# Kernel tuning notes

Measured on AMD Instinct MI355X. Metric: run time of the kernel, lower is better.

## Reference

```python
import jax, jax.numpy as jnp
import numpy as np

DIM = 1536
N_HEADS = 12
HEAD_DIM = DIM // N_HEADS          # 128
C = HEAD_DIM // 2                  # 64 complex channels
C_F = C - 2 * (C // 3)             # 22
C_H = C // 3                       # 21
C_W = C // 3                       # 21
EPS = 1e-6
MAX_F, MAX_HW = 64, 64


def _rope_table(max_len, c_sub):
    # Wan rope_params: theta_j = 10000^{-j/c_sub}, angle = pos * theta
    inv = 1.0 / (10000.0 ** (np.arange(c_sub, dtype=np.float32) / c_sub))
    ang = np.arange(max_len, dtype=np.float32)[:, None] * inv[None, :]
    return jnp.asarray(np.cos(ang)), jnp.asarray(np.sin(ang))


def setup_inputs() -> dict:
    key = jax.random.key(0)
    ks = jax.random.split(key, 12)
    s = 1.0 / np.sqrt(DIM)
    F_, H_, W_ = 9, 16, 28
    S = F_ * H_ * W_
    x = jax.random.normal(ks[0], (1, S, DIM), dtype=jnp.float32)
    Wq = jax.random.normal(ks[1], (DIM, DIM), dtype=jnp.float32) * s
    Wk = jax.random.normal(ks[2], (DIM, DIM), dtype=jnp.float32) * s
    Wv = jax.random.normal(ks[3], (DIM, DIM), dtype=jnp.float32) * s
    Wo = jax.random.normal(ks[4], (DIM, DIM), dtype=jnp.float32) * s
    bq = jnp.zeros((DIM,), jnp.float32)
    bk = jnp.zeros((DIM,), jnp.float32)
    bv = jnp.zeros((DIM,), jnp.float32)
    bo = jnp.zeros((DIM,), jnp.float32)
    gq = jnp.ones((DIM,), jnp.float32)
    gk = jnp.ones((DIM,), jnp.float32)
    cos_f, sin_f = _rope_table(MAX_F, C_F)
    cos_h, sin_h = _rope_table(MAX_HW, C_H)
    cos_w, sin_w = _rope_table(MAX_HW, C_W)
    return dict(x=x, Wq=Wq, bq=bq, Wk=Wk, bk=bk, Wv=Wv, bv=bv, Wo=Wo, bo=bo,
                gq=gq, gk=gk, cos_f=cos_f, sin_f=sin_f, cos_h=cos_h,
                sin_h=sin_h, cos_w=cos_w, sin_w=sin_w, F=F_, H=H_, W=W_)


def _rms(t, g):
    t = t.astype(jnp.float32)
    return t * jax.lax.rsqrt(jnp.mean(t * t, axis=-1, keepdims=True) + EPS) * g


def _grid_cos_sin(cos_f, sin_f, cos_h, sin_h, cos_w, sin_w, F, H, W):
    # concat per-axis angle tables expanded over the (F,H,W) grid -> [S, C]
    def expand(tab, shape):
        return jnp.broadcast_to(tab.reshape(shape + (tab.shape[-1],)), (F, H, W, tab.shape[-1]))
    cos = jnp.concatenate([expand(cos_f[:F], (F, 1, 1)),
                           expand(cos_h[:H], (1, H, 1)),
                           expand(cos_w[:W], (1, 1, W))], axis=-1).reshape(F * H * W, C)
    sin = jnp.concatenate([expand(sin_f[:F], (F, 1, 1)),
                           expand(sin_h[:H], (1, H, 1)),
                           expand(sin_w[:W], (1, 1, W))], axis=-1).reshape(F * H * W, C)
    return cos, sin


def _rope(t, cos, sin):
    # t: [B,S,N,D]; adjacent pairs (even=real, odd=imag) rotated by complex freqs
    b, s, n, d = t.shape
    tr = t.reshape(b, s, n, C, 2)
    e, o = tr[..., 0], tr[..., 1]
    co = cos[None, :, None, :]
    si = sin[None, :, None, :]
    return jnp.stack([e * co - o * si, e * si + o * co], axis=-1).reshape(b, s, n, d)


def reference(x, Wq, bq, Wk, bk, Wv, bv, Wo, bo, gq, gk,
              cos_f, sin_f, cos_h, sin_h, cos_w, sin_w, F, H, W):
    b, s, dim = x.shape
    q = _rms(x @ Wq.T + bq, gq).reshape(b, s, N_HEADS, HEAD_DIM)
    k = _rms(x @ Wk.T + bk, gk).reshape(b, s, N_HEADS, HEAD_DIM)
    v = (x @ Wv.T + bv).reshape(b, s, N_HEADS, HEAD_DIM)
    cos, sin = _grid_cos_sin(cos_f, sin_f, cos_h, sin_h, cos_w, sin_w, F, H, W)
    rq = _rope(q, cos, sin)
    rk = _rope(k, cos, sin)
    scale = 1.0 / jnp.sqrt(jnp.asarray(HEAD_DIM, jnp.float32))
    scores = jnp.einsum('bqhd,bkhd->bhqk', rq, rk) * scale
    att = jax.nn.softmax(scores, axis=-1)
    out = jnp.einsum('bhqk,bkhd->bqhd', att, v).reshape(b, s, dim)
    return out @ Wo.T + bo
```

## Files before the change

kernel.cpp:

```cpp
#include <hip/hip_runtime.h>
#include <math.h>

using u16 = unsigned short;
using u32 = unsigned int;

typedef __attribute__((ext_vector_type(8))) short short8;
typedef __attribute__((ext_vector_type(4))) float float4v;

#define S_LEN 4032
#define DIM   1536
#define NH    12
#define HD    128
#define F_DIM 9
#define H_DIM 16
#define W_DIM 28
#define NX4 1548288
#define NW4 589824

__device__ __forceinline__ float b2f(u16 v) {
  return __uint_as_float(((u32)v) << 16);
}
__device__ __forceinline__ u16 f2bf(float f) {
  u32 u = __float_as_uint(f);
  u32 r = (u + 0x7FFFu + ((u >> 16) & 1u)) >> 16;
  return (u16)r;
}
__device__ __forceinline__ u32 pack2(float lo, float hi) {
  return __builtin_amdgcn_perm(__float_as_uint(hi), __float_as_uint(lo),
                               0x07060302u);
}

__device__ __forceinline__ void gld16(const void* g, void* l) {
  __builtin_amdgcn_global_load_lds(
      (const __attribute__((address_space(1))) void*)g,
      (__attribute__((address_space(3))) void*)l, 16, 0, 0);
}

__device__ __forceinline__ void plswap(u32 a, u32 b, u32& x, u32& y, int lane) {
#if __has_builtin(__builtin_amdgcn_permlane32_swap) && __has_builtin(__builtin_amdgcn_permlane16_swap)
  auto t = __builtin_amdgcn_permlane32_swap(a, b, false, false);
  auto u = __builtin_amdgcn_permlane16_swap(t[0], t[1], false, false);
  x = u[0]; y = u[1];
#else
  u32 ax = (u32)__shfl_xor((int)a, 32, 64), bx = (u32)__shfl_xor((int)b, 32, 64);
  u32 t0 = (lane & 32) ? bx : a;
  u32 t1 = (lane & 32) ? b : ax;
  u32 t0x = (u32)__shfl_xor((int)t0, 16, 64), t1x = (u32)__shfl_xor((int)t1, 16, 64);
  x = (lane & 16) ? t1x : t0;
  y = (lane & 16) ? t1 : t0x;
#endif
}

__global__ void __launch_bounds__(256) cast_all(
    const float* __restrict__ x, const float* __restrict__ wq,
    const float* __restrict__ wk, const float* __restrict__ wv,
    u16* __restrict__ xb, u16* __restrict__ wqb,
    u16* __restrict__ wkb, u16* __restrict__ wvb)
{
  int i = blockIdx.x * 256 + threadIdx.x;
  const float* s; u16* d; int j;
  if (i < NX4)              { s = x;  d = xb;  j = i; }
  else if (i < NX4 + NW4)   { s = wq; d = wqb; j = i - NX4; }
  else if (i < NX4 + 2*NW4) { s = wk; d = wkb; j = i - NX4 - NW4; }
  else                      { s = wv; d = wvb; j = i - NX4 - 2*NW4; }
  const float4 v = ((const float4*)s)[j];
  ushort4 o;
  o.x = f2bf(v.x); o.y = f2bf(v.y); o.z = f2bf(v.z); o.w = f2bf(v.w);
  ((ushort4*)d)[j] = o;
}

__global__ void __launch_bounds__(256) cast_f32_bf16(
    const float* __restrict__ s, u16* __restrict__ d, int n4)
{
  int i = blockIdx.x * 256 + threadIdx.x;
  if (i < n4) {
    const float4 v = ((const float4*)s)[i];
    ushort4 o;
    o.x = f2bf(v.x); o.y = f2bf(v.y); o.z = f2bf(v.z); o.w = f2bf(v.w);
    ((ushort4*)d)[i] = o;
  }
}

template <bool F32OUT>
__device__ __forceinline__ void gemm_core(
    const u16* __restrict__ A, const u16* __restrict__ Bw,
    const float* __restrict__ bias, void* __restrict__ OutV,
    int bm, int bn)
{
  __shared__ u16 As[128 * 64];
  __shared__ u16 Bs[128 * 64];
  const int tid  = threadIdx.x;
  const int wave = tid >> 6, lane = tid & 63;
  const int quad = lane >> 4, l15 = lane & 15;
  const int wm = wave >> 1, wn = wave & 1;

  float4v acc[4][4] = {};

  const int arow = lane >> 3;
  const int acol = (lane & 7) * 8;

  for (int kt = 0; kt < DIM; kt += 64) {
#pragma unroll
    for (int c = 0; c < 4; ++c) {
      int seg = wave * 4 + c;
      int row = seg * 8 + arow;
      int ga = bm + row; if (ga > S_LEN - 1) ga = S_LEN - 1;
      gld16(&A[(size_t)ga * DIM + kt + acol], &As[seg * 512]);
      gld16(&Bw[(size_t)(bn + row) * DIM + kt + acol], &Bs[seg * 512]);
    }
    __syncthreads();
#pragma unroll
    for (int ks = 0; ks < 64; ks += 32) {
      short8 af[4], bf[4];
#pragma unroll
      for (int mt = 0; mt < 4; ++mt)
        af[mt] = *(const short8*)&As[(wm * 64 + mt * 16 + l15) * 64 + ks + quad * 8];
#pragma unroll
      for (int nt = 0; nt < 4; ++nt)
        bf[nt] = *(const short8*)&Bs[(wn * 64 + nt * 16 + l15) * 64 + ks + quad * 8];
#pragma unroll
      for (int mt = 0; mt < 4; ++mt)
#pragma unroll
        for (int nt = 0; nt < 4; ++nt)
          acc[mt][nt] = __builtin_amdgcn_mfma_f32_16x16x32_bf16(af[mt], bf[nt], acc[mt][nt], 0, 0, 0);
    }
    __syncthreads();
  }

#pragma unroll
  for (int mt = 0; mt < 4; ++mt) {
    const int row = bm + wm * 64 + mt * 16 + quad * 4;
#pragma unroll
    for (int nt = 0; nt < 4; ++nt) {
      const int col = bn + wn * 64 + nt * 16 + l15;
      const float bv = bias[col];
#pragma unroll
      for (int r = 0; r < 4; ++r) {
        float v = acc[mt][nt][r] + bv;
        if (row + r < S_LEN) {
          if (F32OUT) ((float*)OutV)[(size_t)(row + r) * DIM + col] = v;
          else        ((u16*)OutV)[(size_t)(row + r) * DIM + col] = f2bf(v);
        }
      }
    }
  }
}

__global__ void __launch_bounds__(256) gemm_qkv(
    const u16* __restrict__ X,
    const u16* __restrict__ Wq, const u16* __restrict__ Wk, const u16* __restrict__ Wv,
    const float* __restrict__ bq, const float* __restrict__ bk, const float* __restrict__ bv,
    u16* __restrict__ Qb, u16* __restrict__ Kb, u16* __restrict__ Vb)
{
  const int z = blockIdx.z;
  const u16* B    = (z == 0) ? Wq : (z == 1) ? Wk : Wv;
  const float* bi = (z == 0) ? bq : (z == 1) ? bk : bv;
  u16* O          = (z == 0) ? Qb : (z == 1) ? Kb : Vb;
  gemm_core<false>(X, B, bi, O, blockIdx.y * 128, blockIdx.x * 128);
}

__global__ void __launch_bounds__(256) gemm_wo(
    const u16* __restrict__ A, const u16* __restrict__ Wo,
    const float* __restrict__ bo, float* __restrict__ Out)
{
  gemm_core<true>(A, Wo, bo, Out, blockIdx.y * 128, blockIdx.x * 128);
}

__global__ void __launch_bounds__(256) rms_rope(
    u16* Q, u16* K,
    const float* __restrict__ gq, const float* __restrict__ gk,
    const float* __restrict__ cf, const float* __restrict__ sf,
    const float* __restrict__ ch, const float* __restrict__ sh,
    const float* __restrict__ cw, const float* __restrict__ sw)
{
  __shared__ float red[2][4];
  const int s = blockIdx.x;
  const int t = threadIdx.x;
  const int wave = t >> 6, lane = t & 63;
  const size_t rowb = (size_t)s * DIM + t * 6;

  u16 qv[6], kv[6];
#pragma unroll
  for (int j = 0; j < 6; ++j) { qv[j] = Q[rowb + j]; kv[j] = K[rowb + j]; }

  float sq = 0.f, sk = 0.f;
#pragma unroll
  for (int j = 0; j < 6; ++j) {
    float a = b2f(qv[j]); sq += a * a;
    float b = b2f(kv[j]); sk += b * b;
  }
#pragma unroll
  for (int m = 1; m < 64; m <<= 1) {
    sq += __shfl_xor(sq, m, 64);
    sk += __shfl_xor(sk, m, 64);
  }
  if (lane == 0) { red[0][wave] = sq; red[1][wave] = sk; }
  __syncthreads();
  const float tq = red[0][0] + red[0][1] + red[0][2] + red[0][3];
  const float tk = red[1][0] + red[1][1] + red[1][2] + red[1][3];
  const float scq = rsqrtf(tq * (1.0f / DIM) + 1e-6f);
  const float sck = rsqrtf(tk * (1.0f / DIM) + 1e-6f);

  const int f  = s / (H_DIM * W_DIM);
  const int hh = (s / W_DIM) % H_DIM;
  const int w  = s % W_DIM;

#pragma unroll
  for (int j = 0; j < 3; ++j) {
    const int pi = t * 3 + j;
    const int c = pi & 63;
    float co, si;
    if (c < 22)      { co = cf[f * 22 + c];        si = sf[f * 22 + c]; }
    else if (c < 43) { co = ch[hh * 21 + c - 22];  si = sh[hh * 21 + c - 22]; }
    else             { co = cw[w * 21 + c - 43];   si = sw[w * 21 + c - 43]; }
    const int gi = 2 * pi;
    const size_t base = (size_t)s * DIM + gi;
    {
      float e = b2f(qv[2 * j])     * scq * gq[gi];
      float o = b2f(qv[2 * j + 1]) * scq * gq[gi + 1];
      Q[base]     = f2bf(e * co - o * si);
      Q[base + 1] = f2bf(e * si + o * co);
    }
    {
      float e = b2f(kv[2 * j])     * sck * gk[gi];
      float o = b2f(kv[2 * j + 1]) * sck * gk[gi + 1];
      K[base]     = f2bf(e * co - o * si);
      K[base + 1] = f2bf(e * si + o * co);
    }
  }
}

__global__ void __launch_bounds__(256) transpose_v(
    const u16* __restrict__ V, u16* __restrict__ Vt)
{
  __shared__ u16 tile[64][65];
  const int s0 = blockIdx.x * 64, d0 = blockIdx.y * 64;
  const int t = threadIdx.x;
#pragma unroll
  for (int i = 0; i < 16; ++i) {
    int idx = t + i * 256; int rr = idx >> 6, cc = idx & 63;
    tile[rr][cc] = V[(size_t)(s0 + rr) * DIM + d0 + cc];
  }
  __syncthreads();
#pragma unroll
  for (int i = 0; i < 16; ++i) {
    int idx = t + i * 256; int rr = idx >> 6, cc = idx & 63;
    Vt[(size_t)(d0 + rr) * S_LEN + s0 + cc] = tile[cc][rr];
  }
}

__global__ void __launch_bounds__(256, 3) attn_kernel(
    const u16* __restrict__ rq, const u16* __restrict__ rk,
    const u16* __restrict__ vt,
    u16* __restrict__ po, float* __restrict__ pl, int klen)
{
  __shared__ u16 Ks[64 * 128];
  __shared__ u16 Vs[128 * 64];

  const int id    = blockIdx.x;
  const int xcd   = id & 7;
  const int band  = id >> 8;
  const int slot  = (id >> 3) & 31;
  const int slice = band * 8 + xcd;
  const int h     = slice % NH;
  const int split = slice / NH;
  const int k_begin = split * klen;
  const int k_end   = (k_begin + klen < S_LEN) ? (k_begin + klen) : S_LEN;
  const int qb = slot * 128;
  const int tid = threadIdx.x, wave = tid >> 6, lane = tid & 63;
  const int quad = lane >> 4, l15 = lane & 15;
  const int q0 = qb + wave * 32;

  const int kr_l   = (lane >> 4);
  const int kc_l   = lane & 15;
  const int vdr_l  = (lane >> 3);
  const int vc_l   = lane & 7;

  short8 qf[2][4];
#pragma unroll
  for (int mt = 0; mt < 2; ++mt) {
    int row = q0 + mt * 16 + l15; if (row > S_LEN - 1) row = S_LEN - 1;
#pragma unroll
    for (int c = 0; c < 4; ++c)
      qf[mt][c] = *(const short8*)&rq[(size_t)row * DIM + h * HD + c * 32 + quad * 8];
  }

  float4v o[2][8] = {};
  float l_[2] = {0.f, 0.f};

  const float SC = 0.08838834764831845f * 1.4426950408889634f;
  const float M0 = 20.0f;

#pragma unroll
  for (int c = 0; c < 4; ++c) {
    const int seg = wave * 4 + c;
    const int kr = seg * 4 + kr_l;
    gld16(&rk[(size_t)(k_begin + kr) * DIM + h * HD + ((kc_l ^ (kr & 15)) << 3)],
          &Ks[seg * 512]);
  }
  __syncthreads();

  for (int kt = k_begin; kt < k_end; kt += 64) {
#pragma unroll
    for (int c = 0; c < 4; ++c) {
      const int seg = wave * 4 + c;
      const int vd = seg * 8 + vdr_l;
      gld16(&vt[(size_t)(h * HD + vd) * S_LEN + kt + ((vc_l ^ (vd & 7)) << 3)],
            &Vs[seg * 512]);
    }

    short8 pf[2][2];

#pragma unroll
    for (int half = 0; half < 2; ++half) {
      float4v sc[2][2] = {};
      __builtin_amdgcn_s_setprio(1);
#pragma unroll
      for (int nth = 0; nth < 2; ++nth) {
        const int krow = (half * 2 + nth) * 16 + l15;
#pragma unroll
        for (int c = 0; c < 4; ++c) {
          const short8 kf = *(const short8*)((char*)Ks + krow * 256 + (((c * 4 + quad) ^ l15) << 4));
          sc[0][nth] = __builtin_amdgcn_mfma_f32_16x16x32_bf16(kf, qf[0][c], sc[0][nth], 0, 0, 0);
          sc[1][nth] = __builtin_amdgcn_mfma_f32_16x16x32_bf16(kf, qf[1][c], sc[1][nth], 0, 0, 0);
        }
      }
      __builtin_amdgcn_s_setprio(0);

#pragma unroll
      for (int mt = 0; mt < 2; ++mt) {
        u32 W[2][2];
#pragma unroll
        for (int nth = 0; nth < 2; ++nth) {
          const float p0 = __builtin_amdgcn_exp2f(fmaf(sc[mt][nth][0], SC, -M0));
          const float p1 = __builtin_amdgcn_exp2f(fmaf(sc[mt][nth][1], SC, -M0));
          const float p2 = __builtin_amdgcn_exp2f(fmaf(sc[mt][nth][2], SC, -M0));
          const float p3 = __builtin_amdgcn_exp2f(fmaf(sc[mt][nth][3], SC, -M0));
          l_[mt] += (p0 + p1) + (p2 + p3);
          W[nth][0] = pack2(p0, p1);
          W[nth][1] = pack2(p2, p3);
        }
        u32 w0, w1, w2, w3;
        plswap(W[0][0], W[1][0], w0, w2, lane);
        plswap(W[0][1], W[1][1], w1, w3, lane);
        union { u32 w[4]; short8 s; } cv;
        cv.w[0] = w0; cv.w[1] = w1; cv.w[2] = w2; cv.w[3] = w3;
        pf[mt][half] = cv.s;
      }
    }

    __syncthreads();

    if (kt + 64 < k_end) {
#pragma unroll
      for (int c = 0; c < 4; ++c) {
        const int seg = wave * 4 + c;
        const int kr = seg * 4 + kr_l;
        gld16(&rk[(size_t)(kt + 64 + kr) * DIM + h * HD + ((kc_l ^ (kr & 15)) << 3)],
              &Ks[seg * 512]);
      }
    }

    __builtin_amdgcn_s_setprio(1);
#pragma unroll
    for (int dt = 0; dt < 8; ++dt) {
      const int drow = dt * 16 + l15;
#pragma unroll
      for (int ko = 0; ko < 2; ++ko) {
        const short8 vf = *(const short8*)((char*)Vs + drow * 128 + (((ko * 4 + quad) ^ (l15 & 7)) << 4));
#pragma unroll
        for (int mt = 0; mt < 2; ++mt)
          o[mt][dt] = __builtin_amdgcn_mfma_f32_16x16x32_bf16(vf, pf[mt][ko], o[mt][dt], 0, 0, 0);
      }
    }
    __builtin_amdgcn_s_setprio(0);

    __syncthreads();
  }

#pragma unroll
  for (int mt = 0; mt < 2; ++mt) {
    float t = l_[mt];
    t += __shfl_xor(t, 16, 64);
    t += __shfl_xor(t, 32, 64);
    l_[mt] = t;
  }
#pragma unroll
  for (int mt = 0; mt < 2; ++mt) {
    const int q = q0 + mt * 16 + l15;
    const bool valid = q < S_LEN;
    const size_t rbase = ((size_t)(split * NH + h) * S_LEN + q) * HD;
#pragma unroll
    for (int dt = 0; dt < 8; ++dt) {
      if (valid) {
        ushort4 pk;
        pk.x = f2bf(o[mt][dt][0]); pk.y = f2bf(o[mt][dt][1]);
        pk.z = f2bf(o[mt][dt][2]); pk.w = f2bf(o[mt][dt][3]);
        *(ushort4*)&po[rbase + dt * 16 + quad * 4] = pk;
      }
    }
    if (quad == 0 && valid)
      pl[(size_t)(split * NH + h) * S_LEN + q] = l_[mt];
  }
}

__global__ void __launch_bounds__(256) attn_merge(
    const u16* __restrict__ po, const float* __restrict__ pl,
    u16* __restrict__ ao, int nsplit)
{
  const int gw = (blockIdx.x * 256 + threadIdx.x) >> 6;
  const int lane = threadIdx.x & 63;
  const int h = gw / S_LEN;
  const int q = gw - h * S_LEN;
  float den = 0.f, a0 = 0.f, a1 = 0.f;
  for (int s = 0; s < nsplit; ++s) {
    const size_t r = (size_t)(s * NH + h) * S_LEN + q;
    den += pl[r];
    const ushort2 v = *(const ushort2*)&po[r * HD + lane * 2];
    a0 += b2f(v.x); a1 += b2f(v.y);
  }
  const float inv = (den > 0.f) ? (1.0f / den) : 0.f;
  ushort2 out;
  out.x = f2bf(a0 * inv);
  out.y = f2bf(a1 * inv);
  *(ushort2*)&ao[(size_t)q * DIM + h * HD + lane * 2] = out;
}

extern "C" void kernel_launch(void* const* d_in, const int* in_sizes, int n_in,
                              void* d_out, int out_size, void* d_ws, size_t ws_size,
                              hipStream_t stream) {
  const float* x  = (const float*)d_in[0];
  const float* Wq = (const float*)d_in[1];
  const float* bq = (const float*)d_in[2];
  const float* Wk = (const float*)d_in[3];
  const float* bk = (const float*)d_in[4];
  const float* Wv = (const float*)d_in[5];
  const float* bv = (const float*)d_in[6];
  const float* Wo = (const float*)d_in[7];
  const float* bo = (const float*)d_in[8];
  const float* gq = (const float*)d_in[9];
  const float* gk = (const float*)d_in[10];
  const float* cf = (const float*)d_in[11];
  const float* sf = (const float*)d_in[12];
  const float* ch = (const float*)d_in[13];
  const float* sh = (const float*)d_in[14];
  const float* cw = (const float*)d_in[15];
  const float* sw = (const float*)d_in[16];

  char* ws = (char*)d_ws;
  const size_t sz  = (size_t)S_LEN * DIM * 2;
  const size_t wsz = (size_t)DIM * DIM * 2;
  u16* Xb  = (u16*)(ws);
  u16* Qb  = (u16*)(ws + sz);
  u16* Kb  = (u16*)(ws + 2 * sz);
  u16* Vb  = (u16*)(ws + 3 * sz);
  u16* Wqb = (u16*)(ws + 4 * sz);
  u16* Wkb = (u16*)(ws + 4 * sz + wsz);
  u16* Wvb = (u16*)(ws + 4 * sz + 2 * wsz);

  const int nsplit = 2;
  const int klen   = 2048;
  const size_t po_one = (size_t)NH * S_LEN * HD * 2;
  char* pbase = ws + 4 * sz + wsz;
  u16*   po = (u16*)pbase;
  float* pl = (float*)(pbase + (size_t)nsplit * po_one);
  u16* Vt  = Xb;
  u16* Ao  = Qb;

  const int nW = DIM * DIM / 4;
  cast_all<<<(NX4 + 3 * NW4) / 256, 256, 0, stream>>>(x, Wq, Wk, Wv, Xb, Wqb, Wkb, Wvb);

  gemm_qkv<<<dim3(12, 32, 3), 256, 0, stream>>>(Xb, Wqb, Wkb, Wvb, bq, bk, bv, Qb, Kb, Vb);

  cast_f32_bf16<<<(nW + 255) / 256, 256, 0, stream>>>(Wo, Wqb, nW);

  rms_rope<<<S_LEN, 256, 0, stream>>>(Qb, Kb, gq, gk, cf, sf, ch, sh, cw, sw);
  transpose_v<<<dim3(63, 24), 256, 0, stream>>>(Vb, Vt);
  attn_kernel<<<384 * nsplit, 256, 0, stream>>>(Qb, Kb, Vt, po, pl, klen);
  attn_merge<<<(NH * S_LEN) / 4, 256, 0, stream>>>(po, pl, Ao, nsplit);
  gemm_wo<<<dim3(12, 32), 256, 0, stream>>>(Ao, Wqb, bo, (float*)d_out);
}
```

Measured before the change: 465.0 us.

## Enlarge attention query tile to 192 rows, fold Wo cast, vectorize rms_rope

```diff
diff --git a/kernel.cpp b/kernel.cpp
--- a/kernel.cpp
+++ b/kernel.cpp
@@ -54,31 +54,22 @@
 __global__ void __launch_bounds__(256) cast_all(
     const float* __restrict__ x, const float* __restrict__ wq,
     const float* __restrict__ wk, const float* __restrict__ wv,
+    const float* __restrict__ wo,
     u16* __restrict__ xb, u16* __restrict__ wqb,
-    u16* __restrict__ wkb, u16* __restrict__ wvb)
+    u16* __restrict__ wkb, u16* __restrict__ wvb,
+    u16* __restrict__ wob)
 {
   int i = blockIdx.x * 256 + threadIdx.x;
   const float* s; u16* d; int j;
   if (i < NX4)              { s = x;  d = xb;  j = i; }
   else if (i < NX4 + NW4)   { s = wq; d = wqb; j = i - NX4; }
   else if (i < NX4 + 2*NW4) { s = wk; d = wkb; j = i - NX4 - NW4; }
-  else                      { s = wv; d = wvb; j = i - NX4 - 2*NW4; }
+  else if (i < NX4 + 3*NW4) { s = wv; d = wvb; j = i - NX4 - 2*NW4; }
+  else                      { s = wo; d = wob; j = i - NX4 - 3*NW4; }
   const float4 v = ((const float4*)s)[j];
   ushort4 o;
   o.x = f2bf(v.x); o.y = f2bf(v.y); o.z = f2bf(v.z); o.w = f2bf(v.w);
   ((ushort4*)d)[j] = o;
-}
-
-__global__ void __launch_bounds__(256) cast_f32_bf16(
-    const float* __restrict__ s, u16* __restrict__ d, int n4)
-{
-  int i = blockIdx.x * 256 + threadIdx.x;
-  if (i < n4) {
-    const float4 v = ((const float4*)s)[i];
-    ushort4 o;
-    o.x = f2bf(v.x); o.y = f2bf(v.y); o.z = f2bf(v.z); o.w = f2bf(v.w);
-    ((ushort4*)d)[i] = o;
-  }
 }
 
 template <bool F32OUT>
@@ -179,15 +170,19 @@
   const int wave = t >> 6, lane = t & 63;
   const size_t rowb = (size_t)s * DIM + t * 6;
 
-  u16 qv[6], kv[6];
-#pragma unroll
-  for (int j = 0; j < 6; ++j) { qv[j] = Q[rowb + j]; kv[j] = K[rowb + j]; }
+  u32* q32 = (u32*)(Q + rowb);
+  u32* k32 = (u32*)(K + rowb);
+  u32 qw[3], kw[3];
+#pragma unroll
+  for (int j = 0; j < 3; ++j) { qw[j] = q32[j]; kw[j] = k32[j]; }
 
   float sq = 0.f, sk = 0.f;
 #pragma unroll
-  for (int j = 0; j < 6; ++j) {
-    float a = b2f(qv[j]); sq += a * a;
-    float b = b2f(kv[j]); sk += b * b;
+  for (int j = 0; j < 3; ++j) {
+    float a0 = b2f((u16)qw[j]), a1 = b2f((u16)(qw[j] >> 16));
+    float b0 = b2f((u16)kw[j]), b1 = b2f((u16)(kw[j] >> 16));
+    sq += a0 * a0 + a1 * a1;
+    sk += b0 * b0 + b1 * b1;
   }
 #pragma unroll
   for (int m = 1; m < 64; m <<= 1) {
@@ -214,18 +209,17 @@
     else if (c < 43) { co = ch[hh * 21 + c - 22];  si = sh[hh * 21 + c - 22]; }
     else             { co = cw[w * 21 + c - 43];   si = sw[w * 21 + c - 43]; }
     const int gi = 2 * pi;
-    const size_t base = (size_t)s * DIM + gi;
+    const float2 gqv = *(const float2*)&gq[gi];
+    const float2 gkv = *(const float2*)&gk[gi];
     {
-      float e = b2f(qv[2 * j])     * scq * gq[gi];
-      float o = b2f(qv[2 * j + 1]) * scq * gq[gi + 1];
-      Q[base]     = f2bf(e * co - o * si);
-      Q[base + 1] = f2bf(e * si + o * co);
+      float e = b2f((u16)qw[j])         * scq * gqv.x;
+      float o = b2f((u16)(qw[j] >> 16)) * scq * gqv.y;
+      q32[j] = (u32)f2bf(e * co - o * si) | ((u32)f2bf(e * si + o * co) << 16);
     }
     {
-      float e = b2f(kv[2 * j])     * sck * gk[gi];
-      float o = b2f(kv[2 * j + 1]) * sck * gk[gi + 1];
-      K[base]     = f2bf(e * co - o * si);
-      K[base + 1] = f2bf(e * si + o * co);
+      float e = b2f((u16)kw[j])         * sck * gkv.x;
+      float o = b2f((u16)(kw[j] >> 16)) * sck * gkv.y;
+      k32[j] = (u32)f2bf(e * co - o * si) | ((u32)f2bf(e * si + o * co) << 16);
     }
   }
 }
@@ -249,7 +243,7 @@
   }
 }
 
-__global__ void __launch_bounds__(256, 3) attn_kernel(
+__global__ void __launch_bounds__(256, 2) attn_kernel(
     const u16* __restrict__ rq, const u16* __restrict__ rk,
     const u16* __restrict__ vt,
     u16* __restrict__ po, float* __restrict__ pl, int klen)
@@ -259,34 +253,35 @@
 
   const int id    = blockIdx.x;
   const int xcd   = id & 7;
-  const int band  = id >> 8;
-  const int slot  = (id >> 3) & 31;
+  const int rest  = id >> 3;
+  const int band  = rest / 21;
+  const int slot  = rest - band * 21;
   const int slice = band * 8 + xcd;
   const int h     = slice % NH;
   const int split = slice / NH;
   const int k_begin = split * klen;
   const int k_end   = (k_begin + klen < S_LEN) ? (k_begin + klen) : S_LEN;
-  const int qb = slot * 128;
+  const int qb = slot * 192;
   const int tid = threadIdx.x, wave = tid >> 6, lane = tid & 63;
   const int quad = lane >> 4, l15 = lane & 15;
-  const int q0 = qb + wave * 32;
+  const int q0 = qb + wave * 48;
 
   const int kr_l   = (lane >> 4);
   const int kc_l   = lane & 15;
   const int vdr_l  = (lane >> 3);
   const int vc_l   = lane & 7;
 
-  short8 qf[2][4];
-#pragma unroll
-  for (int mt = 0; mt < 2; ++mt) {
+  short8 qf[3][4];
+#pragma unroll
+  for (int mt = 0; mt < 3; ++mt) {
     int row = q0 + mt * 16 + l15; if (row > S_LEN - 1) row = S_LEN - 1;
 #pragma unroll
     for (int c = 0; c < 4; ++c)
       qf[mt][c] = *(const short8*)&rq[(size_t)row * DIM + h * HD + c * 32 + quad * 8];
   }
 
-  float4v o[2][8] = {};
-  float l_[2] = {0.f, 0.f};
+  float4v o[3][8] = {};
+  float l_[3] = {0.f, 0.f, 0.f};
 
   const float SC = 0.08838834764831845f * 1.4426950408889634f;
   const float M0 = 20.0f;
@@ -309,11 +304,11 @@
             &Vs[seg * 512]);
     }
 
-    short8 pf[2][2];
+    short8 pf[3][2];
 
 #pragma unroll
     for (int half = 0; half < 2; ++half) {
-      float4v sc[2][2] = {};
+      float4v sc[3][2] = {};
       __builtin_amdgcn_s_setprio(1);
 #pragma unroll
       for (int nth = 0; nth < 2; ++nth) {
@@ -321,14 +316,15 @@
 #pragma unroll
         for (int c = 0; c < 4; ++c) {
           const short8 kf = *(const short8*)((char*)Ks + krow * 256 + (((c * 4 + quad) ^ l15) << 4));
-          sc[0][nth] = __builtin_amdgcn_mfma_f32_16x16x32_bf16(kf, qf[0][c], sc[0][nth], 0, 0, 0);
-          sc[1][nth] = __builtin_amdgcn_mfma_f32_16x16x32_bf16(kf, qf[1][c], sc[1][nth], 0, 0, 0);
+#pragma unroll
+          for (int mt = 0; mt < 3; ++mt)
+            sc[mt][nth] = __builtin_amdgcn_mfma_f32_16x16x32_bf16(kf, qf[mt][c], sc[mt][nth], 0, 0, 0);
         }
       }
       __builtin_amdgcn_s_setprio(0);
 
 #pragma unroll
-      for (int mt = 0; mt < 2; ++mt) {
+      for (int mt = 0; mt < 3; ++mt) {
         u32 W[2][2];
 #pragma unroll
         for (int nth = 0; nth < 2; ++nth) {
@@ -369,7 +365,7 @@
       for (int ko = 0; ko < 2; ++ko) {
         const short8 vf = *(const short8*)((char*)Vs + drow * 128 + (((ko * 4 + quad) ^ (l15 & 7)) << 4));
 #pragma unroll
-        for (int mt = 0; mt < 2; ++mt)
+        for (int mt = 0; mt < 3; ++mt)
           o[mt][dt] = __builtin_amdgcn_mfma_f32_16x16x32_bf16(vf, pf[mt][ko], o[mt][dt], 0, 0, 0);
       }
     }
@@ -379,14 +375,14 @@
   }
 
 #pragma unroll
-  for (int mt = 0; mt < 2; ++mt) {
+  for (int mt = 0; mt < 3; ++mt) {
     float t = l_[mt];
     t += __shfl_xor(t, 16, 64);
     t += __shfl_xor(t, 32, 64);
     l_[mt] = t;
   }
 #pragma unroll
-  for (int mt = 0; mt < 2; ++mt) {
+  for (int mt = 0; mt < 3; ++mt) {
     const int q = q0 + mt * 16 + l15;
     const bool valid = q < S_LEN;
     const size_t rbase = ((size_t)(split * NH + h) * S_LEN + q) * HD;
@@ -461,22 +457,22 @@
   const int nsplit = 2;
   const int klen   = 2048;
   const size_t po_one = (size_t)NH * S_LEN * HD * 2;
-  char* pbase = ws + 4 * sz + wsz;
+  const size_t pl_one = (size_t)NH * S_LEN * 4;
+  char* pbase = ws + 4 * sz;
   u16*   po = (u16*)pbase;
   float* pl = (float*)(pbase + (size_t)nsplit * po_one);
+  u16* Wob = (u16*)(ws + 4 * sz + (size_t)nsplit * (po_one + pl_one));
   u16* Vt  = Xb;
   u16* Ao  = Qb;
 
-  const int nW = DIM * DIM / 4;
-  cast_all<<<(NX4 + 3 * NW4) / 256, 256, 0, stream>>>(x, Wq, Wk, Wv, Xb, Wqb, Wkb, Wvb);
+  cast_all<<<(NX4 + 4 * NW4) / 256, 256, 0, stream>>>(
+      x, Wq, Wk, Wv, Wo, Xb, Wqb, Wkb, Wvb, Wob);
 
   gemm_qkv<<<dim3(12, 32, 3), 256, 0, stream>>>(Xb, Wqb, Wkb, Wvb, bq, bk, bv, Qb, Kb, Vb);
-
-  cast_f32_bf16<<<(nW + 255) / 256, 256, 0, stream>>>(Wo, Wqb, nW);
 
   rms_rope<<<S_LEN, 256, 0, stream>>>(Qb, Kb, gq, gk, cf, sf, ch, sh, cw, sw);
   transpose_v<<<dim3(63, 24), 256, 0, stream>>>(Vb, Vt);
-  attn_kernel<<<384 * nsplit, 256, 0, stream>>>(Qb, Kb, Vt, po, pl, klen);
+  attn_kernel<<<504, 256, 0, stream>>>(Qb, Kb, Vt, po, pl, klen);
   attn_merge<<<(NH * S_LEN) / 4, 256, 0, stream>>>(po, pl, Ao, nsplit);
-  gemm_wo<<<dim3(12, 32), 256, 0, stream>>>(Ao, Wqb, bo, (float*)d_out);
-}
+  gemm_wo<<<dim3(12, 32), 256, 0, stream>>>(Ao, Wob, bo, (float*)d_out);
+}
```

Result: faster. 427.5 us (-8.0%).
